# Kernel tuning notes

Measured on AMD Instinct MI355X. Metric: run time of the kernel, lower is better.

Reference implementation:

```python
import jax, jax.numpy as jnp
import numpy as np

S = 2048        # seqlen_sum (packed tokens)
DIM = 4096
N_HEADS = 32
N_KV_HEADS = 8
HEAD_DIM = 128
ROPE_THETA = 10000.0


def setup_inputs() -> dict:
    key = jax.random.key(0)
    ks = jax.random.split(key, 5)
    x = jax.random.normal(ks[0], (S, DIM), dtype=jnp.float32)
    # true RoPE frequencies: freqs_cis = exp(i * pos * theta^{-2j/d})
    inv_freq = ROPE_THETA ** (-jnp.arange(0, HEAD_DIM, 2, dtype=jnp.float32) / HEAD_DIM)  # [64]
    angles = jnp.arange(S, dtype=jnp.float32)[:, None] * inv_freq[None, :]               # [S,64]
    freqs_cos = jnp.cos(angles)
    freqs_sin = jnp.sin(angles)
    scale = 0.02
    wq = jax.random.normal(ks[1], (DIM, N_HEADS * HEAD_DIM), dtype=jnp.float32) * scale
    wk = jax.random.normal(ks[2], (DIM, N_KV_HEADS * HEAD_DIM), dtype=jnp.float32) * scale
    wv = jax.random.normal(ks[3], (DIM, N_KV_HEADS * HEAD_DIM), dtype=jnp.float32) * scale
    wo = jax.random.normal(ks[4], (N_HEADS * HEAD_DIM, DIM), dtype=jnp.float32) * scale
    return {"x": x, "freqs_cos": freqs_cos, "freqs_sin": freqs_sin,
            "wq": wq, "wk": wk, "wv": wv, "wo": wo}


def _apply_rope(t, cos, sin):
    # t: [S, H, D]; pairs (t0,t1) along last dim form complex numbers (torch view_as_complex)
    tr = t.reshape(t.shape[0], t.shape[1], -1, 2)
    t0, t1 = tr[..., 0], tr[..., 1]
    c = cos[:, None, :]  # [S,1,D/2]
    s = sin[:, None, :]
    o0 = t0 * c - t1 * s
    o1 = t0 * s + t1 * c
    return jnp.stack([o0, o1], axis=-1).reshape(t.shape)


def reference(x, freqs_cos, freqs_sin, wq, wk, wv, wo):
    repeats = N_HEADS // N_KV_HEADS
    xq = (x @ wq).reshape(S, N_HEADS, HEAD_DIM)
    xk = (x @ wk).reshape(S, N_KV_HEADS, HEAD_DIM)
    xv = (x @ wv).reshape(S, N_KV_HEADS, HEAD_DIM)
    xq = _apply_rope(xq, freqs_cos, freqs_sin)
    xk = _apply_rope(xk, freqs_cos, freqs_sin)
    # GQA: repeat_interleave KV heads (cache=None path -> key/val = xk/xv)
    key = jnp.repeat(xk, repeats, axis=1)  # [S, N_HEADS, D]
    val = jnp.repeat(xv, repeats, axis=1)
    scale = HEAD_DIM ** -0.5
    scores = jnp.einsum('qhd,khd->hqk', xq, key) * scale   # [H,S,S]
    attn = jax.nn.softmax(scores, axis=-1)
    out = jnp.einsum('hqk,khd->qhd', attn, val)            # [S,H,D]
    return out.reshape(S, N_HEADS * HEAD_DIM) @ wo
```

## Files before the change

### kernel.cpp

```cpp
#include <hip/hip_runtime.h>

#define S_LEN 2048
#define DIM   4096
#define NH    32
#define NKV   8
#define HD    128
#define QKV_LD 6144
#define KOFF 4096
#define VOFF 5120

typedef __attribute__((ext_vector_type(8))) __bf16 bf16x8;
typedef __attribute__((ext_vector_type(4))) float  floatx4;

union U8 { unsigned short u[8]; bf16x8 v; int4 i4; };

__device__ inline unsigned short f2bf(float f) {
  unsigned int u = __float_as_uint(f);
  u += 0x7fff + ((u >> 16) & 1);
  return (unsigned short)(u >> 16);
}
__device__ inline float bf2f(unsigned short h) {
  return __uint_as_float(((unsigned int)h) << 16);
}

__device__ inline floatx4 mfma16(bf16x8 a, bf16x8 b, floatx4 c) {
  return __builtin_amdgcn_mfma_f32_16x16x32_bf16(a, b, c, 0, 0, 0);
}

typedef __attribute__((address_space(1))) void GV;
typedef __attribute__((address_space(3))) void LV;
__device__ inline void gload_lds16(const unsigned short* g, unsigned short* l) {
  __builtin_amdgcn_global_load_lds((GV*)g, (LV*)l, 16, 0, 0);
}

__global__ __launch_bounds__(256) void transpose_cvt(
    const float* __restrict__ in, unsigned short* __restrict__ outT, int K, int N)
{
  __shared__ float t[32][33];
  const int n0 = blockIdx.x * 32, k0 = blockIdx.y * 32;
  const int tx = threadIdx.x & 31, ty = threadIdx.x >> 5;
#pragma unroll
  for (int i = 0; i < 32; i += 8)
    t[ty + i][tx] = in[(size_t)(k0 + ty + i) * N + n0 + tx];
  __syncthreads();
#pragma unroll
  for (int i = 0; i < 32; i += 8)
    outT[(size_t)(n0 + ty + i) * K + k0 + tx] = f2bf(t[tx][ty + i]);
}

__global__ __launch_bounds__(256) void cvt_f32_bf16(
    const float* __restrict__ in, unsigned short* __restrict__ out)
{
  int i = (blockIdx.x * 256 + threadIdx.x) * 8;
  float4 a = *(const float4*)(in + i);
  float4 b = *(const float4*)(in + i + 4);
  U8 t;
  t.u[0] = f2bf(a.x); t.u[1] = f2bf(a.y); t.u[2] = f2bf(a.z); t.u[3] = f2bf(a.w);
  t.u[4] = f2bf(b.x); t.u[5] = f2bf(b.y); t.u[6] = f2bf(b.z); t.u[7] = f2bf(b.w);
  *(int4*)(out + i) = t.i4;
}

template<bool C_F32>
__global__ __launch_bounds__(256) void gemm_bt(
    const unsigned short* __restrict__ A,
    const unsigned short* __restrict__ Bt,
    void* __restrict__ C_, int M, int N, int K)
{
  __shared__ __align__(16) unsigned short As[128 * 32];
  __shared__ __align__(16) unsigned short Bs[128 * 32];

  const int tid  = threadIdx.x;
  const int wave = tid >> 6;
  const int lane = tid & 63;
  const int quad = lane >> 4;
  const int l16  = lane & 15;
  const int m0 = blockIdx.y * 128, n0 = blockIdx.x * 128;
  const int mw = (wave & 1) * 64, nw = (wave >> 1) * 64;

  floatx4 acc[4][4] = {};

  for (int k0 = 0; k0 < K; k0 += 32) {
#pragma unroll
    for (int p = 0; p < 2; p++) {
      int c = wave * 128 + p * 64 + lane;
      gload_lds16(A  + (size_t)(m0 + (c >> 2)) * K + k0 + (c & 3) * 8,
                  As + (wave * 128 + p * 64) * 8);
      gload_lds16(Bt + (size_t)(n0 + (c >> 2)) * K + k0 + (c & 3) * 8,
                  Bs + (wave * 128 + p * 64) * 8);
    }
    __syncthreads();

    bf16x8 af[4], bf[4];
#pragma unroll
    for (int mt = 0; mt < 4; mt++)
      af[mt] = *(const bf16x8*)(As + (mw + mt * 16 + l16) * 32 + quad * 8);
#pragma unroll
    for (int nt = 0; nt < 4; nt++)
      bf[nt] = *(const bf16x8*)(Bs + (nw + nt * 16 + l16) * 32 + quad * 8);
#pragma unroll
    for (int mt = 0; mt < 4; mt++)
#pragma unroll
      for (int nt = 0; nt < 4; nt++)
        acc[mt][nt] = mfma16(af[mt], bf[nt], acc[mt][nt]);
    __syncthreads();
  }

#pragma unroll
  for (int mt = 0; mt < 4; mt++)
#pragma unroll
    for (int nt = 0; nt < 4; nt++)
#pragma unroll
      for (int i = 0; i < 4; i++) {
        int r = m0 + mw + mt * 16 + quad * 4 + i;
        int c = n0 + nw + nt * 16 + l16;
        if (C_F32) ((float*)C_)[(size_t)r * N + c] = acc[mt][nt][i];
        else ((unsigned short*)C_)[(size_t)r * N + c] = f2bf(acc[mt][nt][i]);
      }
}

__global__ __launch_bounds__(256) void rope_kernel(
    unsigned short* __restrict__ qkv,
    const float* __restrict__ fcos, const float* __restrict__ fsin)
{
  int idx = blockIdx.x * 256 + threadIdx.x;
  int p = idx & 63;
  int t = idx >> 6;
  int h = t % (NH + NKV);
  int s = t / (NH + NKV);

  float c  = fcos[s * 64 + p];
  float sn = fsin[s * 64 + p];
  const float qs = 0.08838834764831845f;

  unsigned short* base;
  float m;
  if (h < NH) { base = qkv + (size_t)s * QKV_LD + h * HD + p * 2; m = qs; }
  else { base = qkv + (size_t)s * QKV_LD + KOFF + (h - NH) * HD + p * 2; m = 1.f; }

  unsigned int both = *(const unsigned int*)base;
  float t0 = bf2f((unsigned short)(both & 0xffff));
  float t1 = bf2f((unsigned short)(both >> 16));
  unsigned int o0 = f2bf((t0 * c - t1 * sn) * m);
  unsigned int o1 = f2bf((t0 * sn + t1 * c) * m);
  *(unsigned int*)base = o0 | (o1 << 16);
}

__global__ __launch_bounds__(256) void vtrans_kernel(
    const unsigned short* __restrict__ qkv, unsigned short* __restrict__ vt)
{
  __shared__ unsigned short t[32][34];
  const int s0 = blockIdx.x * 32;
  const int d0 = blockIdx.y * 32;
  const int tx = threadIdx.x & 31, ty = threadIdx.x >> 5;
#pragma unroll
  for (int i = 0; i < 32; i += 8)
    t[ty + i][tx] = qkv[(size_t)(s0 + ty + i) * QKV_LD + VOFF + d0 + tx];
  __syncthreads();
#pragma unroll
  for (int i = 0; i < 32; i += 8)
    vt[(size_t)(d0 + ty + i) * S_LEN + s0 + tx] = t[tx][ty + i];
}

__global__ __launch_bounds__(256, 2) void attn_kernel(
    const unsigned short* __restrict__ qkv,
    const unsigned short* __restrict__ vt,
    unsigned short* __restrict__ o)
{
  __shared__ __align__(16) unsigned short Ks[64 * 136];
  __shared__ __align__(16) unsigned short Vs[128 * 72];
  __shared__ __align__(16) unsigned short Ps[4][2][16 * 72];

  const int h    = blockIdx.x;
  const int qblk = blockIdx.y;
  const int kvh  = h >> 2;
  const int tid  = threadIdx.x;
  const int wave = tid >> 6;
  const int lane = tid & 63;
  const int quad = lane >> 4;
  const int l16  = lane & 15;
  const int qr   = qblk * 128 + wave * 16;

  bf16x8 qf[2][4];
#pragma unroll
  for (int mt = 0; mt < 2; mt++)
#pragma unroll
    for (int ks = 0; ks < 4; ks++)
      qf[mt][ks] = *(const bf16x8*)(qkv + (size_t)(qr + mt * 64 + l16) * QKV_LD
                                    + h * HD + ks * 32 + quad * 8);

  floatx4 accO[2][8] = {};
  float l_i[2][4] = {};

  int4 pk[4], pv4[4];
#define LOAD_TILE(kb_) do {                                                     \
    _Pragma("unroll")                                                           \
    for (int j = 0; j < 4; j++) {                                               \
      int c = tid + 256 * j;                                                    \
      pk[j] = *(const int4*)(qkv + (size_t)((kb_) * 64 + (c >> 4)) * QKV_LD     \
                              + KOFF + kvh * HD + (c & 15) * 8);                \
      pv4[j] = *(const int4*)(vt + (size_t)(kvh * HD + (c >> 3)) * S_LEN        \
                              + (kb_) * 64 + (c & 7) * 8);                      \
    } } while (0)
#define STORE_TILE() do {                                                       \
    _Pragma("unroll")                                                           \
    for (int j = 0; j < 4; j++) {                                               \
      int c = tid + 256 * j;                                                    \
      *(int4*)(Ks + (c >> 4) * 136 + (c & 15) * 8) = pk[j];                     \
      *(int4*)(Vs + (c >> 3) * 72 + (c & 7) * 8) = pv4[j];                      \
    } } while (0)

  LOAD_TILE(0);
  STORE_TILE();
  __syncthreads();

  for (int kb = 0; kb < S_LEN / 64; kb++) {
    if (kb + 1 < S_LEN / 64) LOAD_TILE(kb + 1);

    floatx4 sacc[2][4] = {};
#pragma unroll
    for (int ks = 0; ks < 4; ks++)
#pragma unroll
      for (int nt = 0; nt < 4; nt++) {
        bf16x8 kf = *(const bf16x8*)(Ks + (nt * 16 + l16) * 136 + ks * 32 + quad * 8);
        sacc[0][nt] = mfma16(qf[0][ks], kf, sacc[0][nt]);
        sacc[1][nt] = mfma16(qf[1][ks], kf, sacc[1][nt]);
      }

#pragma unroll
    for (int mt = 0; mt < 2; mt++)
#pragma unroll
      for (int nt = 0; nt < 4; nt++)
#pragma unroll
        for (int i = 0; i < 4; i++) {
          float pv = __expf(sacc[mt][nt][i]);
          l_i[mt][i] += pv;
          Ps[wave][mt][(quad * 4 + i) * 72 + nt * 16 + l16] = f2bf(pv);
        }

#pragma unroll
    for (int k2 = 0; k2 < 2; k2++) {
      bf16x8 pf0 = *(const bf16x8*)(Ps[wave][0] + l16 * 72 + k2 * 32 + quad * 8);
      bf16x8 pf1 = *(const bf16x8*)(Ps[wave][1] + l16 * 72 + k2 * 32 + quad * 8);
#pragma unroll
      for (int dt = 0; dt < 8; dt++) {
        bf16x8 vf = *(const bf16x8*)(Vs + (dt * 16 + l16) * 72 + k2 * 32 + quad * 8);
        accO[0][dt] = mfma16(pf0, vf, accO[0][dt]);
        accO[1][dt] = mfma16(pf1, vf, accO[1][dt]);
      }
    }
    __syncthreads();
    if (kb + 1 < S_LEN / 64) {
      STORE_TILE();
      __syncthreads();
    }
  }

#pragma unroll
  for (int off = 1; off < 16; off <<= 1)
#pragma unroll
    for (int mt = 0; mt < 2; mt++)
#pragma unroll
      for (int i = 0; i < 4; i++) l_i[mt][i] += __shfl_xor(l_i[mt][i], off, 64);

#pragma unroll
  for (int mt = 0; mt < 2; mt++)
#pragma unroll
    for (int dt = 0; dt < 8; dt++)
#pragma unroll
      for (int i = 0; i < 4; i++) {
        float val = accO[mt][dt][i] / l_i[mt][i];
        o[(size_t)(qr + mt * 64 + quad * 4 + i) * (NH * HD) + h * HD + dt * 16 + l16]
            = f2bf(val);
      }
#undef LOAD_TILE
#undef STORE_TILE
}

extern "C" void kernel_launch(void* const* d_in, const int* in_sizes, int n_in,
                              void* d_out, int out_size, void* d_ws, size_t ws_size,
                              hipStream_t stream)
{
  const float* x    = (const float*)d_in[0];
  const float* fcos = (const float*)d_in[1];
  const float* fsin = (const float*)d_in[2];
  const float* wq   = (const float*)d_in[3];
  const float* wk   = (const float*)d_in[4];
  const float* wv   = (const float*)d_in[5];
  const float* wo   = (const float*)d_in[6];
  float* out = (float*)d_out;

  unsigned short* ws = (unsigned short*)d_ws;
  unsigned short* xb   = ws;
  unsigned short* wT   = xb   + (size_t)S_LEN * DIM;
  unsigned short* woT  = wT   + (size_t)QKV_LD * DIM;
  unsigned short* qkv  = woT  + (size_t)DIM * (NH * HD);
  unsigned short* vt   = qkv  + (size_t)S_LEN * QKV_LD;
  unsigned short* attn = vt   + (size_t)S_LEN * (NKV * HD);

  cvt_f32_bf16<<<(S_LEN * DIM) / (256 * 8), 256, 0, stream>>>(x, xb);
  transpose_cvt<<<dim3(DIM / 32, DIM / 32),        256, 0, stream>>>(wq, wT, DIM, DIM);
  transpose_cvt<<<dim3((NKV * HD) / 32, DIM / 32), 256, 0, stream>>>(wk, wT + (size_t)KOFF * DIM, DIM, NKV * HD);
  transpose_cvt<<<dim3((NKV * HD) / 32, DIM / 32), 256, 0, stream>>>(wv, wT + (size_t)VOFF * DIM, DIM, NKV * HD);
  transpose_cvt<<<dim3(DIM / 32, (NH * HD) / 32),  256, 0, stream>>>(wo, woT, NH * HD, DIM);

  gemm_bt<false><<<dim3(QKV_LD / 128, S_LEN / 128), 256, 0, stream>>>(xb, wT, qkv, S_LEN, QKV_LD, DIM);

  rope_kernel<<<(S_LEN * (NH + NKV) * 64) / 256, 256, 0, stream>>>(qkv, fcos, fsin);
  vtrans_kernel<<<dim3(S_LEN / 32, (NKV * HD) / 32), 256, 0, stream>>>(qkv, vt);

  attn_kernel<<<dim3(NH, S_LEN / 128), 256, 0, stream>>>(qkv, vt, attn);

  gemm_bt<true><<<dim3(DIM / 128, S_LEN / 128), 256, 0, stream>>>(attn, woT, out, S_LEN, DIM, NH * HD);
}
```

Measured before the change: 643.1 us.

## Double-buffer K/V tiles and pass P via lane shuffles instead of LDS

Adds a second shared-memory buffer for K and V so the next tile is stored while the current one is consumed, leaving one barrier per iteration instead of two. Swaps the MFMA operand order so scores come out transposed, which lets the softmax probabilities be packed into bf16 pairs and redistributed through cross-lane shuffles. This removes the per-wave P round trip through shared memory. It also raises wave priority around the MFMA blocks and simplifies the row-sum reduction. The cost is more LDS per block, which may lower occupancy, plus extra shuffle instructions.

```diff
diff --git a/kernel.cpp b/kernel.cpp
--- a/kernel.cpp
+++ b/kernel.cpp
@@ -13,6 +13,7 @@
 typedef __attribute__((ext_vector_type(4))) float  floatx4;
 
 union U8 { unsigned short u[8]; bf16x8 v; int4 i4; };
+union U32x4 { unsigned int u[4]; bf16x8 v; };
 
 __device__ inline unsigned short f2bf(float f) {
   unsigned int u = __float_as_uint(f);
@@ -166,18 +167,17 @@
     const unsigned short* __restrict__ vt,
     unsigned short* __restrict__ o)
 {
-  __shared__ __align__(16) unsigned short Ks[64 * 136];
-  __shared__ __align__(16) unsigned short Vs[128 * 72];
-  __shared__ __align__(16) unsigned short Ps[4][2][16 * 72];
+  __shared__ __align__(16) unsigned short Ks[2][64 * 136];
+  __shared__ __align__(16) unsigned short Vs[2][128 * 72];
 
   const int h    = blockIdx.x;
   const int qblk = blockIdx.y;
   const int kvh  = h >> 2;
   const int tid  = threadIdx.x;
-  const int wave = tid >> 6;
   const int lane = tid & 63;
   const int quad = lane >> 4;
   const int l16  = lane & 15;
+  const int wave = tid >> 6;
   const int qr   = qblk * 128 + wave * 16;
 
   bf16x8 qf[2][4];
@@ -189,7 +189,7 @@
                                     + h * HD + ks * 32 + quad * 8);
 
   floatx4 accO[2][8] = {};
-  float l_i[2][4] = {};
+  float l_i[2] = {0.f, 0.f};
 
   int4 pk[4], pv4[4];
 #define LOAD_TILE(kb_) do {                                                     \
@@ -201,77 +201,112 @@
       pv4[j] = *(const int4*)(vt + (size_t)(kvh * HD + (c >> 3)) * S_LEN        \
                               + (kb_) * 64 + (c & 7) * 8);                      \
     } } while (0)
-#define STORE_TILE() do {                                                       \
+#define STORE_TILE(b_) do {                                                     \
     _Pragma("unroll")                                                           \
     for (int j = 0; j < 4; j++) {                                               \
       int c = tid + 256 * j;                                                    \
-      *(int4*)(Ks + (c >> 4) * 136 + (c & 15) * 8) = pk[j];                     \
-      *(int4*)(Vs + (c >> 3) * 72 + (c & 7) * 8) = pv4[j];                      \
+      *(int4*)(Ks[b_] + (c >> 4) * 136 + (c & 15) * 8) = pk[j];                 \
+      *(int4*)(Vs[b_] + (c >> 3) * 72 + (c & 7) * 8) = pv4[j];                  \
     } } while (0)
 
   LOAD_TILE(0);
-  STORE_TILE();
+  STORE_TILE(0);
   __syncthreads();
 
+  const int srcA = ((quad & 1) << 5) | l16;
+  const bool hi  = (quad & 2);
+
   for (int kb = 0; kb < S_LEN / 64; kb++) {
+    const int cur = kb & 1;
     if (kb + 1 < S_LEN / 64) LOAD_TILE(kb + 1);
 
+    const unsigned short* Ksc = Ks[cur];
+    const unsigned short* Vsc = Vs[cur];
+
     floatx4 sacc[2][4] = {};
+    __builtin_amdgcn_s_setprio(1);
 #pragma unroll
     for (int ks = 0; ks < 4; ks++)
 #pragma unroll
       for (int nt = 0; nt < 4; nt++) {
-        bf16x8 kf = *(const bf16x8*)(Ks + (nt * 16 + l16) * 136 + ks * 32 + quad * 8);
-        sacc[0][nt] = mfma16(qf[0][ks], kf, sacc[0][nt]);
-        sacc[1][nt] = mfma16(qf[1][ks], kf, sacc[1][nt]);
-      }
-
-#pragma unroll
-    for (int mt = 0; mt < 2; mt++)
-#pragma unroll
-      for (int nt = 0; nt < 4; nt++)
-#pragma unroll
-        for (int i = 0; i < 4; i++) {
-          float pv = __expf(sacc[mt][nt][i]);
-          l_i[mt][i] += pv;
-          Ps[wave][mt][(quad * 4 + i) * 72 + nt * 16 + l16] = f2bf(pv);
-        }
+        bf16x8 kf = *(const bf16x8*)(Ksc + (nt * 16 + l16) * 136 + ks * 32 + quad * 8);
+        sacc[0][nt] = mfma16(kf, qf[0][ks], sacc[0][nt]);
+        sacc[1][nt] = mfma16(kf, qf[1][ks], sacc[1][nt]);
+      }
+    __builtin_amdgcn_s_setprio(0);
+
+    unsigned int wp[2][2][4];
+#pragma unroll
+    for (int mt = 0; mt < 2; mt++) {
+      float ls = 0.f;
+#pragma unroll
+      for (int nt = 0; nt < 4; nt++) {
+        float e0 = __expf(sacc[mt][nt][0]);
+        float e1 = __expf(sacc[mt][nt][1]);
+        float e2 = __expf(sacc[mt][nt][2]);
+        float e3 = __expf(sacc[mt][nt][3]);
+        ls += (e0 + e1) + (e2 + e3);
+        wp[mt][0][nt] = (unsigned int)f2bf(e0) | ((unsigned int)f2bf(e1) << 16);
+        wp[mt][1][nt] = (unsigned int)f2bf(e2) | ((unsigned int)f2bf(e3) << 16);
+      }
+      l_i[mt] += ls;
+    }
 
 #pragma unroll
     for (int k2 = 0; k2 < 2; k2++) {
-      bf16x8 pf0 = *(const bf16x8*)(Ps[wave][0] + l16 * 72 + k2 * 32 + quad * 8);
-      bf16x8 pf1 = *(const bf16x8*)(Ps[wave][1] + l16 * 72 + k2 * 32 + quad * 8);
+      bf16x8 paf[2];
+#pragma unroll
+      for (int mt = 0; mt < 2; mt++) {
+        const int ntl = k2 * 2, nth = k2 * 2 + 1;
+        unsigned int a0 = __shfl((int)wp[mt][0][ntl], srcA, 64);
+        unsigned int b0 = __shfl((int)wp[mt][0][nth], srcA, 64);
+        unsigned int a1 = __shfl((int)wp[mt][1][ntl], srcA, 64);
+        unsigned int b1 = __shfl((int)wp[mt][1][nth], srcA, 64);
+        unsigned int a2 = __shfl((int)wp[mt][0][ntl], srcA + 16, 64);
+        unsigned int b2 = __shfl((int)wp[mt][0][nth], srcA + 16, 64);
+        unsigned int a3 = __shfl((int)wp[mt][1][ntl], srcA + 16, 64);
+        unsigned int b3 = __shfl((int)wp[mt][1][nth], srcA + 16, 64);
+        U32x4 pw;
+        pw.u[0] = hi ? b0 : a0;
+        pw.u[1] = hi ? b1 : a1;
+        pw.u[2] = hi ? b2 : a2;
+        pw.u[3] = hi ? b3 : a3;
+        paf[mt] = pw.v;
+      }
+      __builtin_amdgcn_s_setprio(1);
 #pragma unroll
       for (int dt = 0; dt < 8; dt++) {
-        bf16x8 vf = *(const bf16x8*)(Vs + (dt * 16 + l16) * 72 + k2 * 32 + quad * 8);
-        accO[0][dt] = mfma16(pf0, vf, accO[0][dt]);
-        accO[1][dt] = mfma16(pf1, vf, accO[1][dt]);
-      }
+        bf16x8 vf = *(const bf16x8*)(Vsc + (dt * 16 + l16) * 72 + k2 * 32 + quad * 8);
+        accO[0][dt] = mfma16(paf[0], vf, accO[0][dt]);
+        accO[1][dt] = mfma16(paf[1], vf, accO[1][dt]);
+      }
+      __builtin_amdgcn_s_setprio(0);
     }
+
+    if (kb + 1 < S_LEN / 64) STORE_TILE(cur ^ 1);
     __syncthreads();
-    if (kb + 1 < S_LEN / 64) {
-      STORE_TILE();
-      __syncthreads();
-    }
   }
 
 #pragma unroll
-  for (int off = 1; off < 16; off <<= 1)
-#pragma unroll
-    for (int mt = 0; mt < 2; mt++)
-#pragma unroll
-      for (int i = 0; i < 4; i++) l_i[mt][i] += __shfl_xor(l_i[mt][i], off, 64);
-
-#pragma unroll
-  for (int mt = 0; mt < 2; mt++)
+  for (int mt = 0; mt < 2; mt++) {
+    l_i[mt] += __shfl_xor(l_i[mt], 16, 64);
+    l_i[mt] += __shfl_xor(l_i[mt], 32, 64);
+  }
+
+#pragma unroll
+  for (int mt = 0; mt < 2; mt++) {
+    float lq[4];
+#pragma unroll
+    for (int i = 0; i < 4; i++) lq[i] = __shfl(l_i[mt], quad * 4 + i, 64);
 #pragma unroll
     for (int dt = 0; dt < 8; dt++)
 #pragma unroll
       for (int i = 0; i < 4; i++) {
-        float val = accO[mt][dt][i] / l_i[mt][i];
+        float val = accO[mt][dt][i] / lq[i];
         o[(size_t)(qr + mt * 64 + quad * 4 + i) * (NH * HD) + h * HD + dt * 16 + l16]
             = f2bf(val);
       }
+  }
 #undef LOAD_TILE
 #undef STORE_TILE
 }
```

Result: faster. 567.0 us (-11.8%).
